# Kernel tuning notes

Measured on AMD Instinct MI355X. Metric: run time of the kernel, lower is better.

The kernel has to match this reference:

```python
import jax, jax.numpy as jnp
import numpy as np

HID = 64
EPS = 1e-12  # tf.contrib.layers.layer_norm variance_epsilon


def _ln(x, g, b):
    m = jnp.mean(x, axis=-1, keepdims=True)
    v = jnp.mean(jnp.square(x - m), axis=-1, keepdims=True)
    return (x - m) * jax.lax.rsqrt(v + EPS) * g + b


def setup_inputs() -> dict:
    key = jax.random.key(0)
    k1, k2, k3, k4 = jax.random.split(key, 4)
    N, T, OBS, ACT = 2048, 256, 96, 32
    D = OBS + ACT
    obss = jax.random.normal(k1, (N, T, OBS), dtype=jnp.float32)
    actions = jax.random.normal(k2, (N, T, ACT), dtype=jnp.float32)
    W = jax.random.normal(k3, (D + HID, 4 * HID), dtype=jnp.float32) * (1.0 / np.sqrt(D + HID))
    ln_gamma = jnp.ones((5, HID), dtype=jnp.float32)   # i, j, f, o, state norms
    ln_beta = jnp.zeros((5, HID), dtype=jnp.float32)
    dense_W = jax.random.uniform(k4, (HID, 1), dtype=jnp.float32, minval=-0.003, maxval=0.003)
    dense_b = jnp.zeros((1,), dtype=jnp.float32)
    return {"obss": obss, "actions": actions, "W": W, "ln_gamma": ln_gamma,
            "ln_beta": ln_beta, "dense_W": dense_W, "dense_b": dense_b}


def reference(obss, actions, W, ln_gamma, ln_beta, dense_W, dense_b):
    # [N,T,obs+act] -> time-major [T,N,D]
    x = jnp.concatenate([obss, actions], axis=-1)
    xt = jnp.transpose(x, (1, 0, 2))
    N = x.shape[0]
    c0 = jnp.zeros((N, HID), dtype=x.dtype)
    h0 = jnp.zeros((N, HID), dtype=x.dtype)
    forget_bias = jnp.asarray(1.0, dtype=x.dtype)

    def step(carry, x_t):
        c, h = carry
        z = jnp.concatenate([x_t, h], axis=-1) @ W  # [N, 4*HID], no bias
        i, j, f, o = jnp.split(z, 4, axis=-1)
        i = _ln(i, ln_gamma[0], ln_beta[0])
        j = _ln(j, ln_gamma[1], ln_beta[1])
        f = _ln(f, ln_gamma[2], ln_beta[2])
        o = _ln(o, ln_gamma[3], ln_beta[3])
        new_c = c * jax.nn.sigmoid(f + forget_bias) + jax.nn.sigmoid(i) * jnp.tanh(j)
        new_c = _ln(new_c, ln_gamma[4], ln_beta[4])
        new_h = jnp.tanh(new_c) * jax.nn.sigmoid(o)
        return (new_c, new_h), new_h

    _, hs = jax.lax.scan(step, (c0, h0), xt)  # hs: [T,N,HID]
    outputs = jnp.transpose(hs, (1, 0, 2))     # [N,T,HID]
    q = outputs @ dense_W + dense_b            # [N,T,1]
    return q
```

## Files before the change

### kernel.cpp

```cpp
#include <hip/hip_runtime.h>

#define TT 256
#define OBS 96
#define ACTD 32
#define HID 64
#define RPB 4
#define XHP 200
#define EPS 1e-12f

typedef __bf16 bf16x8 __attribute__((ext_vector_type(8)));
typedef float f32x4 __attribute__((ext_vector_type(4)));
typedef unsigned short u16x8 __attribute__((ext_vector_type(8)));
typedef unsigned int u32;
typedef unsigned short u16;

__device__ __forceinline__ u16 f2bf(float f) {
  u32 x = __builtin_bit_cast(u32, f);
  x += 0x7fffu + ((x >> 16) & 1u);
  return (u16)(x >> 16);
}
__device__ __forceinline__ u32 pk2bf(float a, float b) {
  return (u32)f2bf(a) | ((u32)f2bf(b) << 16);
}
__device__ __forceinline__ float sigm(float x) { return 1.0f / (1.0f + __expf(-x)); }
__device__ __forceinline__ float tanh_(float x) { return 1.0f - 2.0f / (__expf(2.0f * x) + 1.0f); }

template <int CTRL>
__device__ __forceinline__ float dpp_add(float x) {
  int t = __builtin_amdgcn_update_dpp(0, __builtin_bit_cast(int, x), CTRL, 0xF, 0xF, true);
  return x + __builtin_bit_cast(float, t);
}
__device__ __forceinline__ float red16(float x) {
  x = dpp_add<0xB1>(x);
  x = dpp_add<0x4E>(x);
  x = dpp_add<0x124>(x);
  x = dpp_add<0x128>(x);
  return x;
}
__device__ __forceinline__ float red32(float x) {
  x = red16(x);
  x += __shfl_xor(x, 16, 64);
  return x;
}

__global__ __launch_bounds__(256, 2) void lstm_fused(
    const float* __restrict__ obss, const float* __restrict__ actions,
    const float* __restrict__ Wm, const float* __restrict__ gamma,
    const float* __restrict__ beta, const float* __restrict__ dWv,
    const float* __restrict__ dbv, float* __restrict__ out)
{
  __shared__ u16 xh[16 * XHP];
  __shared__ float gates[4][RPB][64];
  __shared__ float cst[RPB][64];

  const int tid = threadIdx.x;
  const int wv = tid >> 6;
  const int ln = tid & 63;
  const int l15 = ln & 15;
  const int quad = ln >> 4;
  const int n0 = blockIdx.x * RPB;

  for (int i = tid; i < 16 * XHP / 2; i += 256) ((u32*)xh)[i] = 0u;
  for (int i = tid; i < RPB * 64; i += 256) ((float*)cst)[i] = 0.0f;

  u16x8 bw[6][4];
  #pragma unroll
  for (int kt = 0; kt < 6; ++kt)
    #pragma unroll
    for (int nt = 0; nt < 4; ++nt)
      #pragma unroll
      for (int j = 0; j < 8; ++j)
        bw[kt][nt][j] = f2bf(Wm[(kt * 32 + quad * 8 + j) * 256 + wv * 64 + nt * 16 + l15]);

  float gg[4], gb[4];
  #pragma unroll
  for (int nt = 0; nt < 4; ++nt) {
    gg[nt] = gamma[wv * 64 + nt * 16 + l15];
    gb[nt] = beta[wv * 64 + nt * 16 + l15];
  }

  const int crow = tid >> 5;
  const int ec = (tid & 31) * 2;
  const float cg0 = gamma[4 * 64 + ec], cg1 = gamma[4 * 64 + ec + 1];
  const float cb0 = beta[4 * 64 + ec],  cb1 = beta[4 * 64 + ec + 1];
  const float dw0 = dWv[ec], dw1 = dWv[ec + 1];
  const float bias = dbv[0];

  const int lt = tid & 127;
  const int xr = lt >> 5;
  const int xq = lt & 31;
  const float* obs_p = obss + (size_t)(n0 + xr) * TT * OBS;
  const float* act_p = actions + (size_t)(n0 + xr) * TT * ACTD;

  __syncthreads();

  if (tid >= 128) {
    f32x4 x0;
    if (xq < 24) x0 = *(const f32x4*)(obs_p + xq * 4);
    else         x0 = *(const f32x4*)(act_p + (xq - 24) * 4);
    u32* dst = (u32*)(xh + xr * XHP + xq * 4);
    dst[0] = pk2bf(x0[0], x0[1]);
    dst[1] = pk2bf(x0[2], x0[3]);
  }
  __syncthreads();

  for (int t = 0; t < TT; ++t) {
    const int tn = (t < TT - 1) ? t + 1 : t;
    f32x4 xnx;
    if (tid >= 128) {
      if (xq < 24) xnx = *(const f32x4*)(obs_p + tn * OBS + xq * 4);
      else         xnx = *(const f32x4*)(act_p + tn * ACTD + (xq - 24) * 4);
    }

    u16x8 af[6];
    #pragma unroll
    for (int kt = 0; kt < 6; ++kt)
      af[kt] = *(const u16x8*)(xh + l15 * XHP + kt * 32 + quad * 8);

    f32x4 acc[4];
    #pragma unroll
    for (int nt = 0; nt < 4; ++nt) {
      f32x4 a = {0.0f, 0.0f, 0.0f, 0.0f};
      #pragma unroll
      for (int kt = 0; kt < 6; ++kt)
        a = __builtin_amdgcn_mfma_f32_16x16x32_bf16(
            __builtin_bit_cast(bf16x8, af[kt]),
            __builtin_bit_cast(bf16x8, bw[kt][nt]), a, 0, 0, 0);
      acc[nt] = a;
    }

    float s[4], ss[4];
    #pragma unroll
    for (int r = 0; r < 4; ++r) {
      s[r]  = acc[0][r] + acc[1][r] + acc[2][r] + acc[3][r];
      ss[r] = acc[0][r] * acc[0][r] + acc[1][r] * acc[1][r] +
              acc[2][r] * acc[2][r] + acc[3][r] * acc[3][r];
      s[r]  = red16(s[r]);
      ss[r] = red16(ss[r]);
    }
    if (ln < 16) {
      #pragma unroll
      for (int r = 0; r < RPB; ++r) {
        const float mean = s[r] * (1.0f / 64.0f);
        const float var  = ss[r] * (1.0f / 64.0f) - mean * mean;
        const float rstd = rsqrtf(var + EPS);
        #pragma unroll
        for (int nt = 0; nt < 4; ++nt)
          gates[wv][r][nt * 16 + l15] = (acc[nt][r] - mean) * rstd * gg[nt] + gb[nt];
      }
    }
    __syncthreads();

    if (tid < 128) {
      const float2 iv = *(const float2*)&gates[0][crow][ec];
      const float2 jv = *(const float2*)&gates[1][crow][ec];
      const float2 fv = *(const float2*)&gates[2][crow][ec];
      const float2 ov = *(const float2*)&gates[3][crow][ec];
      const float2 cv = *(const float2*)&cst[crow][ec];
      const float nc0 = cv.x * sigm(fv.x + 1.0f) + sigm(iv.x) * tanh_(jv.x);
      const float nc1 = cv.y * sigm(fv.y + 1.0f) + sigm(iv.y) * tanh_(jv.y);
      float s2  = red32(nc0 + nc1);
      float ss2 = red32(nc0 * nc0 + nc1 * nc1);
      const float mean = s2 * (1.0f / 64.0f);
      const float var  = ss2 * (1.0f / 64.0f) - mean * mean;
      const float rstd = rsqrtf(var + EPS);
      const float c0 = (nc0 - mean) * rstd * cg0 + cb0;
      const float c1 = (nc1 - mean) * rstd * cg1 + cb1;
      *(float2*)&cst[crow][ec] = make_float2(c0, c1);
      const float h0 = tanh_(c0) * sigm(ov.x);
      const float h1 = tanh_(c1) * sigm(ov.y);
      *(u32*)(xh + crow * XHP + 128 + ec) = pk2bf(h0, h1);

      float qp = red32(h0 * dw0 + h1 * dw1);
      if ((tid & 31) == 0) out[(size_t)(n0 + crow) * TT + t] = qp + bias;
    } else {
      u32* dst = (u32*)(xh + xr * XHP + xq * 4);
      dst[0] = pk2bf(xnx[0], xnx[1]);
      dst[1] = pk2bf(xnx[2], xnx[3]);
    }
    __syncthreads();
  }
}

extern "C" void kernel_launch(void* const* d_in, const int* in_sizes, int n_in,
                              void* d_out, int out_size, void* d_ws, size_t ws_size,
                              hipStream_t stream) {
  const float* obss    = (const float*)d_in[0];
  const float* actions = (const float*)d_in[1];
  const float* Wm      = (const float*)d_in[2];
  const float* gamma   = (const float*)d_in[3];
  const float* beta    = (const float*)d_in[4];
  const float* dWv     = (const float*)d_in[5];
  const float* dbv     = (const float*)d_in[6];
  float* out = (float*)d_out;
  lstm_fused<<<dim3(2048 / RPB), dim3(256), 0, stream>>>(obss, actions, Wm, gamma,
                                                         beta, dWv, dbv, out);
}
```

Baseline: 750.5 us.

## Process 16 rows per block with 512 threads and chunked input prefetch

Raises rows per block from 4 to 16 so the 16x16 MFMA tiles are fully used instead of wasting 12 of 16 rows. Work is split across 8 waves, each computing two 16-column tiles. LayerNorm partial sums are exchanged through shared memory, and the elementwise cell update is spread over 4 waves holding c state in registers. Inputs are prefetched 8 timesteps at a time into a shared-memory chunk, and q outputs are batched and written every 8 steps. The grid shrinks to 128 blocks, which may underfill the GPU's compute units, and the separate gate-normalization stage leaves waves 4-7 idle.

```diff
diff --git a/kernel.cpp b/kernel.cpp
--- a/kernel.cpp
+++ b/kernel.cpp
@@ -3,9 +3,10 @@
 #define TT 256
 #define OBS 96
 #define ACTD 32
-#define HID 64
-#define RPB 4
-#define XHP 200
+#define RPB 16
+#define XCS 136
+#define HS 72
+#define ZS 68
 #define EPS 1e-12f
 
 typedef __bf16 bf16x8 __attribute__((ext_vector_type(8)));
@@ -37,148 +38,177 @@
   x = dpp_add<0x128>(x);
   return x;
 }
-__device__ __forceinline__ float red32(float x) {
-  x = red16(x);
-  x += __shfl_xor(x, 16, 64);
-  return x;
-}
-
-__global__ __launch_bounds__(256, 2) void lstm_fused(
+
+__global__ __launch_bounds__(512, 2) void lstm_fused(
     const float* __restrict__ obss, const float* __restrict__ actions,
     const float* __restrict__ Wm, const float* __restrict__ gamma,
     const float* __restrict__ beta, const float* __restrict__ dWv,
     const float* __restrict__ dbv, float* __restrict__ out)
 {
-  __shared__ u16 xh[16 * XHP];
-  __shared__ float gates[4][RPB][64];
-  __shared__ float cst[RPB][64];
+  __shared__ u16 xchunk[8][RPB][XCS];
+  __shared__ u16 hbuf[RPB][HS];
+  __shared__ float zbuf[4][RPB][ZS];
+  __shared__ float pbuf[4][RPB][2][2];
+  __shared__ float qbuf[RPB][8];
 
   const int tid = threadIdx.x;
   const int wv = tid >> 6;
   const int ln = tid & 63;
   const int l15 = ln & 15;
   const int quad = ln >> 4;
+  const int g = wv & 3;
+  const int half = wv >> 2;
   const int n0 = blockIdx.x * RPB;
 
-  for (int i = tid; i < 16 * XHP / 2; i += 256) ((u32*)xh)[i] = 0u;
-  for (int i = tid; i < RPB * 64; i += 256) ((float*)cst)[i] = 0.0f;
-
-  u16x8 bw[6][4];
+  for (int i = tid; i < RPB * HS / 2; i += 512) ((u32*)hbuf)[i] = 0u;
+
+  u16x8 bw[6][2];
   #pragma unroll
   for (int kt = 0; kt < 6; ++kt)
     #pragma unroll
-    for (int nt = 0; nt < 4; ++nt)
+    for (int nt = 0; nt < 2; ++nt)
       #pragma unroll
       for (int j = 0; j < 8; ++j)
-        bw[kt][nt][j] = f2bf(Wm[(kt * 32 + quad * 8 + j) * 256 + wv * 64 + nt * 16 + l15]);
-
-  float gg[4], gb[4];
-  #pragma unroll
-  for (int nt = 0; nt < 4; ++nt) {
-    gg[nt] = gamma[wv * 64 + nt * 16 + l15];
-    gb[nt] = beta[wv * 64 + nt * 16 + l15];
-  }
-
-  const int crow = tid >> 5;
-  const int ec = (tid & 31) * 2;
-  const float cg0 = gamma[4 * 64 + ec], cg1 = gamma[4 * 64 + ec + 1];
-  const float cb0 = beta[4 * 64 + ec],  cb1 = beta[4 * 64 + ec + 1];
-  const float dw0 = dWv[ec], dw1 = dWv[ec + 1];
+        bw[kt][nt][j] =
+            f2bf(Wm[(kt * 32 + quad * 8 + j) * 256 + g * 64 + half * 32 + nt * 16 + l15]);
+
+  const int crow = (wv & 3) * 4 + quad;
+  const int c0 = l15 * 4;
+  float ggam[4][4], gbet[4][4], cgam[4], cbet[4], dwv[4];
+  #pragma unroll
+  for (int e = 0; e < 4; ++e) {
+    cgam[e] = gamma[4 * 64 + c0 + e];
+    cbet[e] = beta[4 * 64 + c0 + e];
+    dwv[e] = dWv[c0 + e];
+    #pragma unroll
+    for (int gg = 0; gg < 4; ++gg) {
+      ggam[gg][e] = gamma[gg * 64 + c0 + e];
+      gbet[gg][e] = beta[gg * 64 + c0 + e];
+    }
+  }
   const float bias = dbv[0];
 
-  const int lt = tid & 127;
-  const int xr = lt >> 5;
-  const int xq = lt & 31;
-  const float* obs_p = obss + (size_t)(n0 + xr) * TT * OBS;
-  const float* act_p = actions + (size_t)(n0 + xr) * TT * ACTD;
-
+  const int srow = tid >> 5;
+  const int slot = tid & 31;
+  const float* obs_p = obss + (size_t)(n0 + srow) * TT * OBS;
+  const float* act_p = actions + (size_t)(n0 + srow) * TT * ACTD;
+
+  f32x4 xst[8];
+  #pragma unroll
+  for (int s = 0; s < 8; ++s) {
+    int tl = s;
+    xst[s] = (slot < 24) ? *(const f32x4*)(obs_p + tl * OBS + slot * 4)
+                         : *(const f32x4*)(act_p + tl * ACTD + (slot - 24) * 4);
+  }
+  #pragma unroll
+  for (int s = 0; s < 8; ++s)
+    *(uint2*)&xchunk[s][srow][slot * 4] =
+        make_uint2(pk2bf(xst[s][0], xst[s][1]), pk2bf(xst[s][2], xst[s][3]));
+
+  f32x4 cst = {0.0f, 0.0f, 0.0f, 0.0f};
   __syncthreads();
 
-  if (tid >= 128) {
-    f32x4 x0;
-    if (xq < 24) x0 = *(const f32x4*)(obs_p + xq * 4);
-    else         x0 = *(const f32x4*)(act_p + (xq - 24) * 4);
-    u32* dst = (u32*)(xh + xr * XHP + xq * 4);
-    dst[0] = pk2bf(x0[0], x0[1]);
-    dst[1] = pk2bf(x0[2], x0[3]);
-  }
-  __syncthreads();
-
   for (int t = 0; t < TT; ++t) {
-    const int tn = (t < TT - 1) ? t + 1 : t;
-    f32x4 xnx;
-    if (tid >= 128) {
-      if (xq < 24) xnx = *(const f32x4*)(obs_p + tn * OBS + xq * 4);
-      else         xnx = *(const f32x4*)(act_p + tn * ACTD + (xq - 24) * 4);
+    const int tm = t & 7;
+
+    if (tm == 0) {
+      #pragma unroll
+      for (int s = 0; s < 8; ++s) {
+        int tl = t + 8 + s; if (tl > TT - 1) tl = TT - 1;
+        xst[s] = (slot < 24) ? *(const f32x4*)(obs_p + tl * OBS + slot * 4)
+                             : *(const f32x4*)(act_p + tl * ACTD + (slot - 24) * 4);
+      }
+      if (t > 0 && wv >= 4 && wv < 6) {
+        const int j = tid - 256;
+        const int row = j >> 3, tt = j & 7;
+        out[(size_t)(n0 + row) * TT + (t - 8) + tt] = qbuf[row][tt] + bias;
+      }
     }
 
     u16x8 af[6];
     #pragma unroll
-    for (int kt = 0; kt < 6; ++kt)
-      af[kt] = *(const u16x8*)(xh + l15 * XHP + kt * 32 + quad * 8);
-
-    f32x4 acc[4];
-    #pragma unroll
-    for (int nt = 0; nt < 4; ++nt) {
-      f32x4 a = {0.0f, 0.0f, 0.0f, 0.0f};
-      #pragma unroll
-      for (int kt = 0; kt < 6; ++kt)
-        a = __builtin_amdgcn_mfma_f32_16x16x32_bf16(
-            __builtin_bit_cast(bf16x8, af[kt]),
-            __builtin_bit_cast(bf16x8, bw[kt][nt]), a, 0, 0, 0);
-      acc[nt] = a;
+    for (int kt = 0; kt < 4; ++kt)
+      af[kt] = *(const u16x8*)&xchunk[tm][l15][kt * 32 + quad * 8];
+    #pragma unroll
+    for (int kt = 4; kt < 6; ++kt)
+      af[kt] = *(const u16x8*)&hbuf[l15][(kt - 4) * 32 + quad * 8];
+
+    f32x4 acc0 = {0.0f, 0.0f, 0.0f, 0.0f}, acc1 = acc0;
+    #pragma unroll
+    for (int kt = 0; kt < 6; ++kt) {
+      acc0 = __builtin_amdgcn_mfma_f32_16x16x32_bf16(
+          __builtin_bit_cast(bf16x8, af[kt]), __builtin_bit_cast(bf16x8, bw[kt][0]), acc0, 0, 0, 0);
+      acc1 = __builtin_amdgcn_mfma_f32_16x16x32_bf16(
+          __builtin_bit_cast(bf16x8, af[kt]), __builtin_bit_cast(bf16x8, bw[kt][1]), acc1, 0, 0, 0);
     }
 
     float s[4], ss[4];
     #pragma unroll
     for (int r = 0; r < 4; ++r) {
-      s[r]  = acc[0][r] + acc[1][r] + acc[2][r] + acc[3][r];
-      ss[r] = acc[0][r] * acc[0][r] + acc[1][r] * acc[1][r] +
-              acc[2][r] * acc[2][r] + acc[3][r] * acc[3][r];
+      s[r]  = acc0[r] + acc1[r];
+      ss[r] = acc0[r] * acc0[r] + acc1[r] * acc1[r];
       s[r]  = red16(s[r]);
       ss[r] = red16(ss[r]);
     }
-    if (ln < 16) {
-      #pragma unroll
-      for (int r = 0; r < RPB; ++r) {
-        const float mean = s[r] * (1.0f / 64.0f);
-        const float var  = ss[r] * (1.0f / 64.0f) - mean * mean;
+    #pragma unroll
+    for (int r = 0; r < 4; ++r) {
+      const int row = quad * 4 + r;
+      zbuf[g][row][half * 32 + l15]      = acc0[r];
+      zbuf[g][row][half * 32 + 16 + l15] = acc1[r];
+    }
+    if (l15 < 4) {
+      const float sv  = l15 == 0 ? s[0]  : l15 == 1 ? s[1]  : l15 == 2 ? s[2]  : s[3];
+      const float ssv = l15 == 0 ? ss[0] : l15 == 1 ? ss[1] : l15 == 2 ? ss[2] : ss[3];
+      *(float2*)&pbuf[g][quad * 4 + l15][half][0] = make_float2(sv, ssv);
+    }
+    __syncthreads();
+
+    if (wv < 4) {
+      float zc[4][4];
+      #pragma unroll
+      for (int gg = 0; gg < 4; ++gg) {
+        const f32x4 p = *(const f32x4*)&pbuf[gg][crow][0][0];
+        const float mean = (p[0] + p[2]) * (1.0f / 64.0f);
+        const float var  = (p[1] + p[3]) * (1.0f / 64.0f) - mean * mean;
         const float rstd = rsqrtf(var + EPS);
+        const f32x4 z = *(const f32x4*)&zbuf[gg][crow][c0];
         #pragma unroll
-        for (int nt = 0; nt < 4; ++nt)
-          gates[wv][r][nt * 16 + l15] = (acc[nt][r] - mean) * rstd * gg[nt] + gb[nt];
-      }
-    }
-    __syncthreads();
-
-    if (tid < 128) {
-      const float2 iv = *(const float2*)&gates[0][crow][ec];
-      const float2 jv = *(const float2*)&gates[1][crow][ec];
-      const float2 fv = *(const float2*)&gates[2][crow][ec];
-      const float2 ov = *(const float2*)&gates[3][crow][ec];
-      const float2 cv = *(const float2*)&cst[crow][ec];
-      const float nc0 = cv.x * sigm(fv.x + 1.0f) + sigm(iv.x) * tanh_(jv.x);
-      const float nc1 = cv.y * sigm(fv.y + 1.0f) + sigm(iv.y) * tanh_(jv.y);
-      float s2  = red32(nc0 + nc1);
-      float ss2 = red32(nc0 * nc0 + nc1 * nc1);
+        for (int e = 0; e < 4; ++e)
+          zc[gg][e] = (z[e] - mean) * rstd * ggam[gg][e] + gbet[gg][e];
+      }
+      float nc[4];
+      #pragma unroll
+      for (int e = 0; e < 4; ++e)
+        nc[e] = cst[e] * sigm(zc[2][e] + 1.0f) + sigm(zc[0][e]) * tanh_(zc[1][e]);
+      float s2  = red16(nc[0] + nc[1] + nc[2] + nc[3]);
+      float ss2 = red16(nc[0] * nc[0] + nc[1] * nc[1] + nc[2] * nc[2] + nc[3] * nc[3]);
       const float mean = s2 * (1.0f / 64.0f);
       const float var  = ss2 * (1.0f / 64.0f) - mean * mean;
       const float rstd = rsqrtf(var + EPS);
-      const float c0 = (nc0 - mean) * rstd * cg0 + cb0;
-      const float c1 = (nc1 - mean) * rstd * cg1 + cb1;
-      *(float2*)&cst[crow][ec] = make_float2(c0, c1);
-      const float h0 = tanh_(c0) * sigm(ov.x);
-      const float h1 = tanh_(c1) * sigm(ov.y);
-      *(u32*)(xh + crow * XHP + 128 + ec) = pk2bf(h0, h1);
-
-      float qp = red32(h0 * dw0 + h1 * dw1);
-      if ((tid & 31) == 0) out[(size_t)(n0 + crow) * TT + t] = qp + bias;
-    } else {
-      u32* dst = (u32*)(xh + xr * XHP + xq * 4);
-      dst[0] = pk2bf(xnx[0], xnx[1]);
-      dst[1] = pk2bf(xnx[2], xnx[3]);
+      float h[4];
+      #pragma unroll
+      for (int e = 0; e < 4; ++e) {
+        const float cn = (nc[e] - mean) * rstd * cgam[e] + cbet[e];
+        cst[e] = cn;
+        h[e] = tanh_(cn) * sigm(zc[3][e]);
+      }
+      *(uint2*)&hbuf[crow][c0] = make_uint2(pk2bf(h[0], h[1]), pk2bf(h[2], h[3]));
+      float qp = red16(h[0] * dwv[0] + h[1] * dwv[1] + h[2] * dwv[2] + h[3] * dwv[3]);
+      if (l15 == 0) qbuf[crow][tm] = qp;
+    }
+    if (tm == 7) {
+      #pragma unroll
+      for (int s = 0; s < 8; ++s)
+        *(uint2*)&xchunk[s][srow][slot * 4] =
+            make_uint2(pk2bf(xst[s][0], xst[s][1]), pk2bf(xst[s][2], xst[s][3]));
     }
     __syncthreads();
+  }
+
+  if (wv >= 4 && wv < 6) {
+    const int j = tid - 256;
+    const int row = j >> 3, tt = j & 7;
+    out[(size_t)(n0 + row) * TT + 248 + tt] = qbuf[row][tt] + bias;
   }
 }
 
@@ -193,6 +223,6 @@
   const float* dWv     = (const float*)d_in[5];
   const float* dbv     = (const float*)d_in[6];
   float* out = (float*)d_out;
-  lstm_fused<<<dim3(2048 / RPB), dim3(256), 0, stream>>>(obss, actions, Wm, gamma,
+  lstm_fused<<<dim3(2048 / RPB), dim3(512), 0, stream>>>(obss, actions, Wm, gamma,
                                                          beta, dWv, dbv, out);
 }
```

New measurement: 697.0 us. -7.1%, faster.
